# Kernel tuning notes

Measured on AMD Instinct MI355X. Metric: run time of the kernel, lower is better.

The kernel has to match this reference:

```python
import jax, jax.numpy as jnp
import numpy as np

H, W = 250, 400
N_RAYS = H * W          # 100000 (one patch)
N_SAMPLES = 1_000_000
P, C, DIM = 50000, 16, 8
STEP_SIZE = 0.005
DENSITY_SHIFT = 0.0
DENSITY_SCALE = min(1.0 / (1.0 - DENSITY_SHIFT), 25.0)


def setup_inputs() -> dict:
    key = jax.random.key(0)
    ks = jax.random.split(key, 12)
    return {
        "trivecs": jax.random.normal(ks[0], (P, C, 3, DIM), dtype=jnp.float32),
        "densities": jax.random.normal(ks[1], (P, C), dtype=jnp.float32),
        "colors": jax.random.normal(ks[2], (P, C, 3), dtype=jnp.float32),
        "local_gweight_s": jax.random.uniform(ks[3], (N_SAMPLES, 3), dtype=jnp.float32),
        "local_gweight_l": jax.random.uniform(ks[4], (N_SAMPLES, 3), dtype=jnp.float32),
        "t_min": jax.random.uniform(ks[5], (N_RAYS,), dtype=jnp.float32),
        "bg": jax.random.uniform(ks[6], (3,), dtype=jnp.float32),
        "local_gindx_s": jax.random.randint(ks[7], (N_SAMPLES, 3), 0, DIM, dtype=jnp.int32),
        "local_gindx_l": jax.random.randint(ks[8], (N_SAMPLES, 3), 0, DIM, dtype=jnp.int32),
        "tensoRF_id": jax.random.randint(ks[9], (N_SAMPLES,), 0, P, dtype=jnp.int32),
        "ray_id": jnp.sort(jax.random.randint(ks[10], (N_SAMPLES,), 0, N_RAYS, dtype=jnp.int32)),
        "step_id": jax.random.randint(ks[11], (N_SAMPLES,), 0, 200, dtype=jnp.int32),
    }


def reference(trivecs, densities, colors, local_gweight_s, local_gweight_l,
              t_min, bg, local_gindx_s, local_gindx_l, tensoRF_id, ray_id, step_id):
    # --- compute_feature: trilinear tensor-decomposition gather ---
    def interp(a):
        vs = trivecs[tensoRF_id, :, a, local_gindx_s[:, a]]  # [N, C]
        vl = trivecs[tensoRF_id, :, a, local_gindx_l[:, a]]  # [N, C]
        return vs * local_gweight_s[:, a:a + 1] + vl * local_gweight_l[:, a:a + 1]

    feature = interp(0) * interp(1) * interp(2)               # [N, C]
    sigma = (feature * densities[tensoRF_id]).sum(axis=1)     # [N]
    color = jnp.einsum('nc,nck->nk', feature, colors[tensoRF_id])  # [N, 3]

    # --- density activation & alpha ---
    density = jax.nn.softplus(sigma - DENSITY_SHIFT * 10.0) * DENSITY_SCALE
    alpha = 1.0 - jnp.exp(-density * STEP_SIZE)               # [N]

    # --- Alphas2Weights: per-ray exclusive transmittance (ray_id sorted) ---
    log_t = -density * STEP_SIZE                              # == log(1 - alpha)
    seg_total = jax.ops.segment_sum(log_t, ray_id, num_segments=N_RAYS)  # [R]
    seg_offset = jnp.concatenate([jnp.zeros((1,), log_t.dtype),
                                  jnp.cumsum(seg_total)[:-1]])           # [R]
    excl = jnp.cumsum(log_t) - log_t - seg_offset[ray_id]     # within-segment excl cumsum
    weights = alpha * jnp.exp(excl)                           # [N]
    bg_weight = jnp.exp(seg_total)                            # [R], prod(1-alpha) per ray

    # --- ray compositing ---
    rgb = jax.nn.sigmoid(color)                               # [N, 3]
    rgb_map = jax.ops.segment_sum(weights[:, None] * rgb, ray_id, num_segments=N_RAYS)
    rgb_map = rgb_map + bg_weight[:, None] * bg[None, :]
    z_val = t_min[ray_id] + step_id.astype(jnp.float32) * STEP_SIZE
    depth_map = jax.ops.segment_sum(weights * z_val, ray_id, num_segments=N_RAYS)
    alpha_map = 1.0 - bg_weight

    rgb_map = rgb_map.T.reshape(3, H, W)
    depth_map = depth_map.reshape(H, W)
    alpha_map = alpha_map.reshape(H, W)
    return rgb_map, depth_map, alpha_map
```

## Files before the change

### kernel.cpp

```cpp
#include <hip/hip_runtime.h>
#include <math.h>

#define HN       250
#define WN       400
#define N_RAYS   (HN * WN)
#define N_SAMP   1000000
#define P_TENSO  50000
#define STEP_SZ  0.005f
#define DENS_SCALE 1.0f
#define NB_SCAN  ((P_TENSO + 1023) / 1024)


#define OFF_PACK    0
#define OFF_RESULTS 32000000
#define OFF_PERM    48000000
#define OFF_IPERM   52000000
#define OFF_COUNTS  56000000
#define OFF_STARTS  56200000
#define OFF_CURSOR  56400000
#define OFF_BSUMS   56600000
#define OFF_RSTART  56601024
#define WS_NEED     (56601024 + 400004 + 64)

#define ROW_STRIDE 20
#define TV_F   (24 * ROW_STRIDE)
#define SLAB_F (TV_F + 16 + 48)

__global__ __launch_bounds__(256) void zero_ints(int* p, int n) {
    int i = blockIdx.x * 256 + threadIdx.x;
    if (i < n) p[i] = 0;
}

__global__ __launch_bounds__(256) void pack_hist_bounds(
    const int*   __restrict__ tenso_id,
    const int*   __restrict__ ray_id,
    const int*   __restrict__ gis, const int* __restrict__ gil,
    const float* __restrict__ gws, const float* __restrict__ gwl,
    int* __restrict__ counts,
    int* __restrict__ ray_start,
    float4* __restrict__ pack)
{
    int n = blockIdx.x * 256 + threadIdx.x;
    if (n >= N_SAMP) return;

    atomicAdd(&counts[tenso_id[n]], 1);

    unsigned bits = (unsigned)gis[n*3+0] | ((unsigned)gis[n*3+1] << 3) | ((unsigned)gis[n*3+2] << 6)
                  | ((unsigned)gil[n*3+0] << 9) | ((unsigned)gil[n*3+1] << 12) | ((unsigned)gil[n*3+2] << 15);
    float4 A = make_float4(gws[n*3+0], gws[n*3+1], gws[n*3+2], gwl[n*3+0]);
    float4 B = make_float4(gwl[n*3+1], gwl[n*3+2], __uint_as_float(bits), 0.0f);
    pack[(size_t)n * 2 + 0] = A;
    pack[(size_t)n * 2 + 1] = B;

    int r = ray_id[n];
    int rprev = (n == 0) ? -1 : ray_id[n - 1];
    for (int q = rprev + 1; q <= r; ++q) ray_start[q] = n;
    if (n == N_SAMP - 1) {
        for (int q = r + 1; q <= N_RAYS; ++q) ray_start[q] = N_SAMP;
    }
}

__global__ __launch_bounds__(256) void scan_local(const int* __restrict__ in,
                                                  int* __restrict__ out,
                                                  int* __restrict__ bsums, int n) {
    __shared__ int lds[256];
    const int t = threadIdx.x;
    const int base = blockIdx.x * 1024;
    int v[4]; int s = 0;
    #pragma unroll
    for (int i = 0; i < 4; ++i) {
        int idx = base + t * 4 + i;
        v[i] = (idx < n) ? in[idx] : 0;
        s += v[i];
    }
    lds[t] = s;
    __syncthreads();
    for (int d = 1; d < 256; d <<= 1) {
        int x = (t >= d) ? lds[t - d] : 0;
        __syncthreads();
        lds[t] += x;
        __syncthreads();
    }
    int run = (t > 0) ? lds[t - 1] : 0;
    #pragma unroll
    for (int i = 0; i < 4; ++i) {
        int idx = base + t * 4 + i;
        if (idx < n) out[idx] = run;
        run += v[i];
    }
    if (t == 255) bsums[blockIdx.x] = lds[255];
}

__global__ __launch_bounds__(64) void scan_totals(int* __restrict__ bsums, int nb) {
    int t = threadIdx.x;
    int v = (t < nb) ? bsums[t] : 0;
    #pragma unroll
    for (int d = 1; d < 64; d <<= 1) {
        int u = __shfl_up(v, d, 64);
        if (t >= d) v += u;
    }
    int excl = __shfl_up(v, 1, 64);
    if (t == 0) excl = 0;
    if (t < nb) bsums[t] = excl;
}

__global__ __launch_bounds__(256) void scan_add(int* __restrict__ starts,
                                                int* __restrict__ cursor,
                                                const int* __restrict__ bsums, int n) {
    int i = blockIdx.x * 256 + threadIdx.x;
    if (i < n) { int v = starts[i] + bsums[i >> 10]; starts[i] = v; cursor[i] = v; }
}

__global__ __launch_bounds__(256) void scatter_perm(
    const int* __restrict__ tenso_id,
    int* __restrict__ cursor,
    int* __restrict__ perm,
    int* __restrict__ iperm)
{
    int n = blockIdx.x * 256 + threadIdx.x;
    if (n >= N_SAMP) return;
    int tid = tenso_id[n];
    int pos = atomicAdd(&cursor[tid], 1);
    perm[pos] = n;
    iperm[n] = pos;
}

__global__ __launch_bounds__(256) void gather_phase(
    const float* __restrict__ trivecs,
    const float* __restrict__ densities,
    const float* __restrict__ colors,
    const int*   __restrict__ starts,
    const int*   __restrict__ counts,
    const int*   __restrict__ perm,
    const float4* __restrict__ pack,
    float* __restrict__ results_f)
{
    __shared__ __align__(16) float lds[4 * SLAB_F];
    const int lane = threadIdx.x & 63;
    const int wv   = threadIdx.x >> 6;
    const int t    = blockIdx.x * 4 + wv;
    if (t >= P_TENSO) return;

    const int start = starts[t];
    const int cnt   = counts[t];
    if (cnt == 0) return;

    float* slab = lds + wv * SLAB_F;
    float* dl   = slab + TV_F;
    float* cl   = dl + 16;

    const float* tvg = trivecs + (size_t)t * 384;
    #pragma unroll
    for (int i = 0; i < 6; ++i) {
        int l = lane + i * 64;
        int c = l / 24;
        int rem = l - c * 24;
        slab[rem * ROW_STRIDE + c] = tvg[l];
    }
    if (lane < 16) dl[lane] = densities[(size_t)t * 16 + lane];
    if (lane < 48) {
        int c = lane / 3, k = lane - c * 3;
        cl[k * 16 + c] = colors[(size_t)t * 48 + lane];
    }

    const int g = lane >> 2;
    const int j = lane & 3;

    const float4 dens4 = *(const float4*)(dl + 4 * j);
    const float4 col0  = *(const float4*)(cl + 4 * j);
    const float4 col1  = *(const float4*)(cl + 16 + 4 * j);
    const float4 col2  = *(const float4*)(cl + 32 + 4 * j);

    const int end = start + cnt;
    const int niter = (cnt + 15) >> 4;

    for (int it = 0; it < niter; ++it) {
        const int pos = start + it * 16 + g;
        const bool valid = (pos < end);
        const int cp = valid ? pos : (end - 1);
        const int n = perm[cp];
        const float4 A = pack[(size_t)n * 2 + 0];
        const float4 B = pack[(size_t)n * 2 + 1];
        const unsigned bits = __float_as_uint(B.z);

        float4 f;
        {
            const int is = bits & 7, il = (bits >> 9) & 7;
            const float4 vs = *(const float4*)(slab + is * ROW_STRIDE + 4 * j);
            const float4 vl = *(const float4*)(slab + il * ROW_STRIDE + 4 * j);
            f.x = vs.x * A.x + vl.x * A.w;
            f.y = vs.y * A.x + vl.y * A.w;
            f.z = vs.z * A.x + vl.z * A.w;
            f.w = vs.w * A.x + vl.w * A.w;
        }
        {
            const int is = (bits >> 3) & 7, il = (bits >> 12) & 7;
            const float4 vs = *(const float4*)(slab + (8 + is) * ROW_STRIDE + 4 * j);
            const float4 vl = *(const float4*)(slab + (8 + il) * ROW_STRIDE + 4 * j);
            f.x *= vs.x * A.y + vl.x * B.x;
            f.y *= vs.y * A.y + vl.y * B.x;
            f.z *= vs.z * A.y + vl.z * B.x;
            f.w *= vs.w * A.y + vl.w * B.x;
        }
        {
            const int is = (bits >> 6) & 7, il = (bits >> 15) & 7;
            const float4 vs = *(const float4*)(slab + (16 + is) * ROW_STRIDE + 4 * j);
            const float4 vl = *(const float4*)(slab + (16 + il) * ROW_STRIDE + 4 * j);
            f.x *= vs.x * A.z + vl.x * B.y;
            f.y *= vs.y * A.z + vl.y * B.y;
            f.z *= vs.z * A.z + vl.z * B.y;
            f.w *= vs.w * A.z + vl.w * B.y;
        }

        float s0 = f.x * dens4.x + f.y * dens4.y + f.z * dens4.z + f.w * dens4.w;
        float s1 = f.x * col0.x  + f.y * col0.y  + f.z * col0.z  + f.w * col0.w;
        float s2 = f.x * col1.x  + f.y * col1.y  + f.z * col1.z  + f.w * col1.w;
        float s3 = f.x * col2.x  + f.y * col2.y  + f.z * col2.z  + f.w * col2.w;

        s0 += __shfl_xor(s0, 1); s0 += __shfl_xor(s0, 2);
        s1 += __shfl_xor(s1, 1); s1 += __shfl_xor(s1, 2);
        s2 += __shfl_xor(s2, 1); s2 += __shfl_xor(s2, 2);
        s3 += __shfl_xor(s3, 1); s3 += __shfl_xor(s3, 2);

        const float sj = (j == 0) ? s0 : (j == 1) ? s1 : (j == 2) ? s2 : s3;
        float val;
        if (j == 0) {
            float dens = fmaxf(sj, 0.0f) + __logf(1.0f + __expf(-fabsf(sj)));
            val = -(dens * DENS_SCALE) * STEP_SZ;
        } else {
            val = 1.0f / (1.0f + __expf(-sj));
        }
        if (valid) results_f[(size_t)pos * 4 + j] = val;
    }
}

__global__ __launch_bounds__(256) void ray_render(
    const float4* __restrict__ results,
    const int*    __restrict__ iperm,
    const float*  __restrict__ t_min,
    const float*  __restrict__ bg,
    const int*    __restrict__ ray_start,
    const int*    __restrict__ step_id,
    float* __restrict__ out)
{
    int r = blockIdx.x * 256 + threadIdx.x;
    if (r >= N_RAYS) return;
    const int s = ray_start[r];
    const int e = ray_start[r + 1];
    const float tmin_r = t_min[r];

    float T = 0.0f, aR = 0.0f, aG = 0.0f, aB = 0.0f, aD = 0.0f;
    for (int n = s; n < e; ++n) {
        const int pos = iperm[n];
        float4 res = results[pos];
        const float lt = res.x;
        const float w = (1.0f - __expf(lt)) * __expf(T);
        T += lt;
        const float z = tmin_r + (float)step_id[n] * STEP_SZ;
        aR += w * res.y;
        aG += w * res.z;
        aB += w * res.w;
        aD += w * z;
    }
    const float bgw = __expf(T);
    out[0 * N_RAYS + r] = aR + bgw * bg[0];
    out[1 * N_RAYS + r] = aG + bgw * bg[1];
    out[2 * N_RAYS + r] = aB + bgw * bg[2];
    out[3 * N_RAYS + r] = aD;
    out[4 * N_RAYS + r] = 1.0f - bgw;
}

__global__ __launch_bounds__(256) void trivec_render_fallback(
    const float* __restrict__ trivecs, const float* __restrict__ densities,
    const float* __restrict__ colors, const float* __restrict__ gws,
    const float* __restrict__ gwl, const float* __restrict__ t_min,
    const float* __restrict__ bg, const int* __restrict__ gis,
    const int* __restrict__ gil, const int* __restrict__ tenso_id,
    const int* __restrict__ ray_id, const int* __restrict__ step_id,
    float* __restrict__ out)
{
    const int lane = threadIdx.x & 63;
    const int r = blockIdx.x * 4 + (threadIdx.x >> 6);
    if (r >= N_RAYS) return;
    const int c = lane & 15;
    const int g = lane >> 4;
    int lo = 0, hi = N_SAMP;
    while (lo < hi) { int mid = (lo + hi) >> 1; if (ray_id[mid] < r) lo = mid + 1; else hi = mid; }
    const int seg_start = lo;
    hi = N_SAMP;
    while (lo < hi) { int mid = (lo + hi) >> 1; if (ray_id[mid] < r + 1) lo = mid + 1; else hi = mid; }
    const int seg_end = lo;
    const float tmin_r = t_min[r];
    float Tlog = 0.0f, accR = 0.0f, accG = 0.0f, accB = 0.0f, accD = 0.0f;
    const int niter = (seg_end - seg_start + 3) >> 2;
    for (int it = 0; it < niter; ++it) {
        const int n = seg_start + it * 4 + g;
        const bool valid = (n < seg_end);
        const int nc = valid ? n : (seg_end - 1);
        const int tid = tenso_id[nc];
        const float* tv = trivecs + (size_t)tid * 384 + c * 24;
        float f = 1.0f;
        #pragma unroll
        for (int a = 0; a < 3; ++a) {
            const int is = gis[nc*3+a], il = gil[nc*3+a];
            const float wS = gws[nc*3+a], wL = gwl[nc*3+a];
            f *= (tv[a*8+is] * wS + tv[a*8+il] * wL);
        }
        const float dns = densities[(size_t)tid * 16 + c];
        const float* colp = colors + ((size_t)tid * 16 + c) * 3;
        float s0 = f*dns, s1 = f*colp[0], s2 = f*colp[1], s3 = f*colp[2];
        #pragma unroll
        for (int m = 1; m < 16; m <<= 1) {
            s0 += __shfl_xor(s0, m); s1 += __shfl_xor(s1, m);
            s2 += __shfl_xor(s2, m); s3 += __shfl_xor(s3, m);
        }
        float dens = fmaxf(s0, 0.0f) + __logf(1.0f + __expf(-fabsf(s0)));
        const float lt = valid ? (-dens * STEP_SZ) : 0.0f;
        const float alpha = 1.0f - __expf(lt);
        const float rr = 1.0f/(1.0f+__expf(-s1)), gg = 1.0f/(1.0f+__expf(-s2)), bb = 1.0f/(1.0f+__expf(-s3));
        const float z = tmin_r + (float)step_id[nc] * STEP_SZ;
        const float lt0 = __shfl(lt,0), lt1 = __shfl(lt,16), lt2 = __shfl(lt,32), lt3 = __shfl(lt,48);
        float excl = Tlog;
        if (g > 0) excl += lt0;
        if (g > 1) excl += lt1;
        if (g > 2) excl += lt2;
        const float w = alpha * __expf(excl);
        Tlog += lt0 + lt1 + lt2 + lt3;
        accR += w*rr; accG += w*gg; accB += w*bb; accD += w*z;
    }
    accR += __shfl_xor(accR,16); accR += __shfl_xor(accR,32);
    accG += __shfl_xor(accG,16); accG += __shfl_xor(accG,32);
    accB += __shfl_xor(accB,16); accB += __shfl_xor(accB,32);
    accD += __shfl_xor(accD,16); accD += __shfl_xor(accD,32);
    const float bgw = __expf(Tlog);
    if (lane == 0) {
        out[0*N_RAYS+r] = accR + bgw*bg[0];
        out[1*N_RAYS+r] = accG + bgw*bg[1];
        out[2*N_RAYS+r] = accB + bgw*bg[2];
        out[3*N_RAYS+r] = accD;
        out[4*N_RAYS+r] = 1.0f - bgw;
    }
}

extern "C" void kernel_launch(void* const* d_in, const int* in_sizes, int n_in,
                              void* d_out, int out_size, void* d_ws, size_t ws_size,
                              hipStream_t stream) {
    const float* trivecs   = (const float*)d_in[0];
    const float* densities = (const float*)d_in[1];
    const float* colors    = (const float*)d_in[2];
    const float* gws       = (const float*)d_in[3];
    const float* gwl       = (const float*)d_in[4];
    const float* t_min     = (const float*)d_in[5];
    const float* bg        = (const float*)d_in[6];
    const int*   gis       = (const int*)d_in[7];
    const int*   gil       = (const int*)d_in[8];
    const int*   tenso_id  = (const int*)d_in[9];
    const int*   ray_id    = (const int*)d_in[10];
    const int*   step_id   = (const int*)d_in[11];
    float* out = (float*)d_out;

    if (ws_size < (size_t)WS_NEED) {
        trivec_render_fallback<<<(N_RAYS + 3) / 4, 256, 0, stream>>>(
            trivecs, densities, colors, gws, gwl, t_min, bg,
            gis, gil, tenso_id, ray_id, step_id, out);
        return;
    }

    char* ws = (char*)d_ws;
    float4* pack     = (float4*)(ws + OFF_PACK);
    float4* results  = (float4*)(ws + OFF_RESULTS);
    int*    perm     = (int*)(ws + OFF_PERM);
    int*    iperm    = (int*)(ws + OFF_IPERM);
    int*    counts   = (int*)(ws + OFF_COUNTS);
    int*    starts   = (int*)(ws + OFF_STARTS);
    int*    cursor   = (int*)(ws + OFF_CURSOR);
    int*    bsums    = (int*)(ws + OFF_BSUMS);
    int*    raystart = (int*)(ws + OFF_RSTART);

    zero_ints<<<(P_TENSO + 255) / 256, 256, 0, stream>>>(counts, P_TENSO);
    pack_hist_bounds<<<(N_SAMP + 255) / 256, 256, 0, stream>>>(
        tenso_id, ray_id, gis, gil, gws, gwl, counts, raystart, pack);
    scan_local<<<NB_SCAN, 256, 0, stream>>>(counts, starts, bsums, P_TENSO);
    scan_totals<<<1, 64, 0, stream>>>(bsums, NB_SCAN);
    scan_add<<<(P_TENSO + 255) / 256, 256, 0, stream>>>(starts, cursor, bsums, P_TENSO);
    scatter_perm<<<(N_SAMP + 255) / 256, 256, 0, stream>>>(tenso_id, cursor, perm, iperm);
    gather_phase<<<(P_TENSO + 3) / 4, 256, 0, stream>>>(
        trivecs, densities, colors, starts, counts, perm, pack, (float*)results);
    ray_render<<<(N_RAYS + 255) / 256, 256, 0, stream>>>(
        results, iperm, t_min, bg, raystart, step_id, out);
}
```

Measured before the change: 336.0 us.

## Fuse counting sort passes: record atomic rank in histogram, single-pass grid-synced scan

The histogram kernel now stores each sample's atomic rank within its tensoRF bucket, so the second atomic scatter pass is replaced by a plain add of start plus rank. The three scan kernels collapse into one kernel that uses a global flag spin barrier across its 49 blocks to combine block sums. A memset replaces the zeroing kernel. This cuts kernel launches and one full pass of atomics over a million samples, at the cost of an extra rank array and a spin barrier that assumes all scan blocks are co-resident.

Result: faster. 284.7 us (-15.2%).

```diff
diff --git a/kernel.cpp b/kernel.cpp
--- a/kernel.cpp
+++ b/kernel.cpp
@@ -15,35 +15,33 @@
 #define OFF_RESULTS 32000000
 #define OFF_PERM    48000000
 #define OFF_IPERM   52000000
-#define OFF_COUNTS  56000000
-#define OFF_STARTS  56200000
-#define OFF_CURSOR  56400000
-#define OFF_BSUMS   56600000
-#define OFF_RSTART  56601024
-#define WS_NEED     (56601024 + 400004 + 64)
+#define OFF_RANK    56000000
+#define OFF_CURSOR  60000000
+#define OFF_STARTS  60200000
+#define OFF_BSUMS   60400000
+#define OFF_FLAG    60400512
+#define OFF_RSTART  60401024
+#define WS_NEED     (60401024 + 400004 + 64)
 
 #define ROW_STRIDE 20
 #define TV_F   (24 * ROW_STRIDE)
 #define SLAB_F (TV_F + 16 + 48)
 
-__global__ __launch_bounds__(256) void zero_ints(int* p, int n) {
-    int i = blockIdx.x * 256 + threadIdx.x;
-    if (i < n) p[i] = 0;
-}
-
-__global__ __launch_bounds__(256) void pack_hist_bounds(
+__global__ __launch_bounds__(256) void pack_bounds_rank(
     const int*   __restrict__ tenso_id,
     const int*   __restrict__ ray_id,
     const int*   __restrict__ gis, const int* __restrict__ gil,
     const float* __restrict__ gws, const float* __restrict__ gwl,
-    int* __restrict__ counts,
+    int* __restrict__ cursor,
+    int* __restrict__ rank,
     int* __restrict__ ray_start,
     float4* __restrict__ pack)
 {
     int n = blockIdx.x * 256 + threadIdx.x;
     if (n >= N_SAMP) return;
 
-    atomicAdd(&counts[tenso_id[n]], 1);
+    const int tid = tenso_id[n];
+    rank[n] = atomicAdd(&cursor[tid], 1);
 
     unsigned bits = (unsigned)gis[n*3+0] | ((unsigned)gis[n*3+1] << 3) | ((unsigned)gis[n*3+2] << 6)
                   | ((unsigned)gil[n*3+0] << 9) | ((unsigned)gil[n*3+1] << 12) | ((unsigned)gil[n*3+2] << 15);
@@ -60,17 +58,22 @@
     }
 }
 
-__global__ __launch_bounds__(256) void scan_local(const int* __restrict__ in,
-                                                  int* __restrict__ out,
-                                                  int* __restrict__ bsums, int n) {
-    __shared__ int lds[256];
+__global__ __launch_bounds__(256) void scan_fused(
+    const int* __restrict__ cursor,
+    int* __restrict__ starts,
+    int* __restrict__ bsums,
+    int* __restrict__ flag)
+{
+    __shared__ int lds[257];
+    const int b = blockIdx.x;
     const int t = threadIdx.x;
-    const int base = blockIdx.x * 1024;
+    const int base = b * 1024 + t * 4;
+
     int v[4]; int s = 0;
     #pragma unroll
     for (int i = 0; i < 4; ++i) {
-        int idx = base + t * 4 + i;
-        v[i] = (idx < n) ? in[idx] : 0;
+        int idx = base + i;
+        v[i] = (idx < P_TENSO) ? cursor[idx] : 0;
         s += v[i];
     }
     lds[t] = s;
@@ -81,48 +84,47 @@
         lds[t] += x;
         __syncthreads();
     }
-    int run = (t > 0) ? lds[t - 1] : 0;
+    if (t == 255) bsums[b] = lds[255];
+
+    __threadfence();
+    __syncthreads();
+    if (t == 0) {
+        atomicAdd(flag, 1);
+        while (atomicAdd(flag, 0) < gridDim.x) { }
+    }
+    __syncthreads();
+    __threadfence();
+
+    if (t < 64) {
+        int x = (t < b) ? bsums[t] : 0;
+        #pragma unroll
+        for (int m = 1; m < 64; m <<= 1) x += __shfl_xor(x, m);
+        if (t == 0) lds[256] = x;
+    }
+    __syncthreads();
+    const int pre = lds[256];
+
+    int run = pre + ((t > 0) ? lds[t - 1] : 0);
     #pragma unroll
     for (int i = 0; i < 4; ++i) {
-        int idx = base + t * 4 + i;
-        if (idx < n) out[idx] = run;
+        int idx = base + i;
+        if (idx < P_TENSO) starts[idx] = run;
         run += v[i];
     }
-    if (t == 255) bsums[blockIdx.x] = lds[255];
-}
-
-__global__ __launch_bounds__(64) void scan_totals(int* __restrict__ bsums, int nb) {
-    int t = threadIdx.x;
-    int v = (t < nb) ? bsums[t] : 0;
-    #pragma unroll
-    for (int d = 1; d < 64; d <<= 1) {
-        int u = __shfl_up(v, d, 64);
-        if (t >= d) v += u;
-    }
-    int excl = __shfl_up(v, 1, 64);
-    if (t == 0) excl = 0;
-    if (t < nb) bsums[t] = excl;
-}
-
-__global__ __launch_bounds__(256) void scan_add(int* __restrict__ starts,
-                                                int* __restrict__ cursor,
-                                                const int* __restrict__ bsums, int n) {
-    int i = blockIdx.x * 256 + threadIdx.x;
-    if (i < n) { int v = starts[i] + bsums[i >> 10]; starts[i] = v; cursor[i] = v; }
-}
-
-__global__ __launch_bounds__(256) void scatter_perm(
+}
+
+__global__ __launch_bounds__(256) void finalize_perm(
     const int* __restrict__ tenso_id,
-    int* __restrict__ cursor,
+    const int* __restrict__ rank,
+    const int* __restrict__ starts,
     int* __restrict__ perm,
     int* __restrict__ iperm)
 {
     int n = blockIdx.x * 256 + threadIdx.x;
     if (n >= N_SAMP) return;
-    int tid = tenso_id[n];
-    int pos = atomicAdd(&cursor[tid], 1);
+    int pos = starts[tenso_id[n]] + rank[n];
+    iperm[n] = pos;
     perm[pos] = n;
-    iperm[n] = pos;
 }
 
 __global__ __launch_bounds__(256) void gather_phase(
@@ -371,21 +373,22 @@
     float4* results  = (float4*)(ws + OFF_RESULTS);
     int*    perm     = (int*)(ws + OFF_PERM);
     int*    iperm    = (int*)(ws + OFF_IPERM);
-    int*    counts   = (int*)(ws + OFF_COUNTS);
+    int*    rank     = (int*)(ws + OFF_RANK);
+    int*    cursor   = (int*)(ws + OFF_CURSOR);
     int*    starts   = (int*)(ws + OFF_STARTS);
-    int*    cursor   = (int*)(ws + OFF_CURSOR);
     int*    bsums    = (int*)(ws + OFF_BSUMS);
+    int*    flag     = (int*)(ws + OFF_FLAG);
     int*    raystart = (int*)(ws + OFF_RSTART);
 
-    zero_ints<<<(P_TENSO + 255) / 256, 256, 0, stream>>>(counts, P_TENSO);
-    pack_hist_bounds<<<(N_SAMP + 255) / 256, 256, 0, stream>>>(
-        tenso_id, ray_id, gis, gil, gws, gwl, counts, raystart, pack);
-    scan_local<<<NB_SCAN, 256, 0, stream>>>(counts, starts, bsums, P_TENSO);
-    scan_totals<<<1, 64, 0, stream>>>(bsums, NB_SCAN);
-    scan_add<<<(P_TENSO + 255) / 256, 256, 0, stream>>>(starts, cursor, bsums, P_TENSO);
-    scatter_perm<<<(N_SAMP + 255) / 256, 256, 0, stream>>>(tenso_id, cursor, perm, iperm);
+    hipMemsetAsync(ws + OFF_CURSOR, 0, (OFF_FLAG + 64) - OFF_CURSOR, stream);
+
+    pack_bounds_rank<<<(N_SAMP + 255) / 256, 256, 0, stream>>>(
+        tenso_id, ray_id, gis, gil, gws, gwl, cursor, rank, raystart, pack);
+    scan_fused<<<NB_SCAN, 256, 0, stream>>>(cursor, starts, bsums, flag);
+    finalize_perm<<<(N_SAMP + 255) / 256, 256, 0, stream>>>(
+        tenso_id, rank, starts, perm, iperm);
     gather_phase<<<(P_TENSO + 3) / 4, 256, 0, stream>>>(
-        trivecs, densities, colors, starts, counts, perm, pack, (float*)results);
+        trivecs, densities, colors, starts, cursor, perm, pack, (float*)results);
     ray_render<<<(N_RAYS + 255) / 256, 256, 0, stream>>>(
         results, iperm, t_min, bg, raystart, step_id, out);
 }
```
